# Kernel tuning notes

Measured on AMD Instinct MI355X. Metric: run time of the kernel, lower is better.

Reference implementation:

```python
import jax, jax.numpy as jnp
import numpy as np
import math

B, Q, H, KVH, D, KV, HID = 2, 1024, 32, 8, 128, 4096, 4096

def rotate_half(x):
    x1, x2 = jnp.split(x, 2, axis=-1)
    return jnp.concatenate([-x2, x1], axis=-1)

def setup_inputs() -> dict:
    key = jax.random.key(0)
    ks = jax.random.split(key, 10)
    inv = 1.0 / math.sqrt(HID)
    return {
        "hidden_states": jax.random.normal(ks[0], (B, Q, HID), dtype=jnp.float32),
        "cos": jax.random.uniform(ks[1], (B, 1, Q, D), dtype=jnp.float32),
        "sin": jax.random.uniform(ks[2], (B, 1, Q, D), dtype=jnp.float32),
        "attention_mask": jnp.zeros((B, 1, Q, KV), dtype=jnp.float32),
        "cache_k": jax.random.normal(ks[3], (B, KVH, KV, D), dtype=jnp.float32),
        "cache_v": jax.random.normal(ks[4], (B, KVH, KV, D), dtype=jnp.float32),
        "sink_ids": jnp.arange(Q, dtype=jnp.int32),
        "Wq": jax.random.normal(ks[5], (H * D, HID), dtype=jnp.float32) * inv,
        "Wk": jax.random.normal(ks[6], (KVH * D, HID), dtype=jnp.float32) * inv,
        "Wv": jax.random.normal(ks[7], (KVH * D, HID), dtype=jnp.float32) * inv,
        "Wo": jax.random.normal(ks[8], (HID, H * D), dtype=jnp.float32) * inv,
    }

def reference(hidden_states, cos, sin, attention_mask, cache_k, cache_v, sink_ids, Wq, Wk, Wv, Wo):
    b, q_len, hid = hidden_states.shape
    d = cos.shape[-1]
    h = Wq.shape[0] // d
    kvh = Wk.shape[0] // d
    n_rep = h // kvh

    # projections -> (b, heads, q, d)
    qs = (hidden_states @ Wq.T).reshape(b, q_len, h, d).transpose(0, 2, 1, 3)
    ks = (hidden_states @ Wk.T).reshape(b, q_len, kvh, d).transpose(0, 2, 1, 3)
    vs = (hidden_states @ Wv.T).reshape(b, q_len, kvh, d).transpose(0, 2, 1, 3)

    # RoPE
    qs = qs * cos + rotate_half(qs) * sin
    ks = ks * cos + rotate_half(ks) * sin

    # sink new K/V into the paged cache at sink_ids, then read back the full cache
    k_cache = cache_k.at[:, :, sink_ids, :].set(ks)
    v_cache = cache_v.at[:, :, sink_ids, :].set(vs)

    # repeat_kv: (b, kvh, kv, d) -> (b, h, kv, d)
    k_full = jnp.repeat(k_cache, n_rep, axis=1)
    v_full = jnp.repeat(v_cache, n_rep, axis=1)

    scores = jnp.einsum('bhqd,bhkd->bhqk', qs, k_full) / math.sqrt(d)
    scores = scores + attention_mask
    attn = jax.nn.softmax(scores.astype(jnp.float32), axis=-1).astype(qs.dtype)
    out = jnp.einsum('bhqk,bhkd->bhqd', attn, v_full)
    out = out.transpose(0, 2, 1, 3).reshape(b, q_len, h * d)
    return out @ Wo.T
```

## Files before the change

### kernel.cpp

```cpp
#include <hip/hip_runtime.h>

typedef __bf16 bf16;
typedef __attribute__((ext_vector_type(8))) __bf16 bf16x8;
typedef __attribute__((ext_vector_type(4))) __bf16 bf16x4;
typedef __attribute__((ext_vector_type(4))) float floatx4;

#define LOG2E 1.4426950408889634f
#define CEXP (0.08838834764831845f * 1.4426950408889634f)

__device__ __forceinline__ void lds16(const void* g, void* l) {
  __builtin_amdgcn_global_load_lds(
      (const __attribute__((address_space(1))) unsigned int*)(unsigned long long)g,
      (__attribute__((address_space(3))) unsigned int*)(unsigned int)(unsigned long long)l,
      16, 0, 0);
}

__device__ __forceinline__ void memfence() { asm volatile("" ::: "memory"); }

template <typename CT>
__global__ __launch_bounds__(256, 2) void gemm_bt(const bf16* __restrict__ A,
                                                  const bf16* __restrict__ W,
                                                  CT* __restrict__ C,
                                                  int M, int N, int K) {
  __shared__ bf16 sA[2][128 * 64];
  __shared__ bf16 sB[2][128 * 64];
  const int tid = threadIdx.x;
  const int lane = tid & 63;
  const int wave = tid >> 6;
  const int quad = lane >> 4;
  const int l16 = lane & 15;
  const int m0 = blockIdx.y * 128;
  const int n0 = blockIdx.x * 128;
  const int wm = (wave >> 1) * 64;
  const int wn = (wave & 1) * 64;

  floatx4 acc[4][4] = {};

  const int rsub = lane >> 3;
  const int csw = ((lane & 7) ^ rsub) * 8;
  const int NT = K >> 6;

  auto stage = [&](int buf, int t) {
    const int k0 = t << 6;
#pragma unroll
    for (int i = 0; i < 4; ++i) {
      const int row = i * 32 + wave * 8 + rsub;
      lds16(A + (long)(m0 + row) * K + k0 + csw, sA[buf] + (i * 32 + wave * 8) * 64);
      lds16(W + (long)(n0 + row) * K + k0 + csw, sB[buf] + (i * 32 + wave * 8) * 64);
    }
  };

  stage(0, 0);
  stage(1, 1);

  for (int t = 0; t < NT - 1; ++t) {
    const int buf = t & 1;
    asm volatile("s_waitcnt vmcnt(8)" ::: "memory");
    __builtin_amdgcn_s_barrier();
    memfence();
#pragma unroll
    for (int s = 0; s < 2; ++s) {
      bf16x8 af[4], bfr[4];
#pragma unroll
      for (int i = 0; i < 4; ++i)
        af[i] = *(const bf16x8*)(sA[buf] + (wm + i * 16 + l16) * 64 +
                                 (((s * 4 + quad) ^ (l16 & 7)) << 3));
#pragma unroll
      for (int j = 0; j < 4; ++j)
        bfr[j] = *(const bf16x8*)(sB[buf] + (wn + j * 16 + l16) * 64 +
                                  (((s * 4 + quad) ^ (l16 & 7)) << 3));
#pragma unroll
      for (int i = 0; i < 4; ++i)
#pragma unroll
        for (int j = 0; j < 4; ++j)
          acc[i][j] = __builtin_amdgcn_mfma_f32_16x16x32_bf16(af[i], bfr[j], acc[i][j], 0, 0, 0);
    }
    memfence();
    __builtin_amdgcn_s_barrier();
    memfence();
    if (t + 2 < NT) stage(buf, t + 2);
  }

  asm volatile("s_waitcnt vmcnt(0)" ::: "memory");
  __builtin_amdgcn_s_barrier();
  memfence();
  {
    const int buf = (NT - 1) & 1;
#pragma unroll
    for (int s = 0; s < 2; ++s) {
      bf16x8 af[4], bfr[4];
#pragma unroll
      for (int i = 0; i < 4; ++i)
        af[i] = *(const bf16x8*)(sA[buf] + (wm + i * 16 + l16) * 64 +
                                 (((s * 4 + quad) ^ (l16 & 7)) << 3));
#pragma unroll
      for (int j = 0; j < 4; ++j)
        bfr[j] = *(const bf16x8*)(sB[buf] + (wn + j * 16 + l16) * 64 +
                                  (((s * 4 + quad) ^ (l16 & 7)) << 3));
#pragma unroll
      for (int i = 0; i < 4; ++i)
#pragma unroll
        for (int j = 0; j < 4; ++j)
          acc[i][j] = __builtin_amdgcn_mfma_f32_16x16x32_bf16(af[i], bfr[j], acc[i][j], 0, 0, 0);
    }
  }

#pragma unroll
  for (int i = 0; i < 4; ++i) {
    const int row = m0 + wm + i * 16 + quad * 4;
#pragma unroll
    for (int j = 0; j < 4; ++j) {
      const int col = n0 + wn + j * 16 + l16;
#pragma unroll
      for (int r = 0; r < 4; ++r)
        C[(long)(row + r) * N + col] = (CT)acc[i][j][r];
    }
  }
}

__global__ __launch_bounds__(256, 2) void attn(const bf16* __restrict__ qr,
                                               const bf16* __restrict__ kc,
                                               const bf16* __restrict__ vt,
                                               const float* __restrict__ mask,
                                               const int* __restrict__ flag,
                                               bf16* __restrict__ o) {
  __shared__ bf16 sK[2][64 * 128];
  __shared__ bf16 sV[2][128 * 64];
  __shared__ bf16 sP[4 * 32 * 64];
  const int tid = threadIdx.x, lane = tid & 63, wave = tid >> 6;
  const int quad = lane >> 4, l16 = lane & 15;

  int id = blockIdx.x;
  const int kvh = id & 7;
  id >>= 3;
  const int b = id & 1;
  id >>= 1;
  const int h = kvh * 4 + (id & 3);
  const int q0 = (id >> 2) * 128;
  const int qw = q0 + wave * 32;

  const bf16* qbase = qr + ((long)(b * 32 + h) * 1024 + qw) * 128;
  bf16x8 qf[2][4];
#pragma unroll
  for (int qt = 0; qt < 2; ++qt)
#pragma unroll
    for (int ks = 0; ks < 4; ++ks)
      qf[qt][ks] = *(const bf16x8*)(qbase + (long)(qt * 16 + l16) * 128 +
                                    ks * 32 + quad * 8);

  floatx4 oacc[8][2] = {};
  floatx4 lrun4[2] = {};

  const bool use_mask = (*flag != 0);
  const bf16* kbase = kc + (long)(b * 8 + kvh) * 4096 * 128;
  const bf16* vbase = vt + (long)(b * 8 + kvh) * 128 * 4096;
  bf16* sPw = sP + wave * 2048;

  auto stage = [&](int buf, int kt) {
    const int kv0 = kt * 64;
#pragma unroll
    for (int it = 0; it < 4; ++it) {
      const int r0 = wave * 16 + it * 4;
      const int row = r0 + (lane >> 4);
      lds16(kbase + (long)(kv0 + row) * 128 + (((lane & 15) ^ (row & 15)) << 3),
            sK[buf] + r0 * 128);
    }
#pragma unroll
    for (int it = 0; it < 4; ++it) {
      const int r0 = wave * 32 + it * 8;
      const int row = r0 + (lane >> 3);
      lds16(vbase + (long)row * 4096 + kv0 + (((lane & 7) ^ (row & 7)) << 3),
            sV[buf] + r0 * 64);
    }
  };

  stage(0, 0);
  __syncthreads();

  for (int kt = 0; kt < 64; ++kt) {
    const int cur = kt & 1;
    const int kv0 = kt * 64;
    if (kt < 63) stage(cur ^ 1, kt + 1);

    floatx4 s[4][2] = {};
    __builtin_amdgcn_s_setprio(1);
#pragma unroll
    for (int ks = 0; ks < 4; ++ks)
#pragma unroll
      for (int j = 0; j < 4; ++j) {
        const bf16x8 kf = *(const bf16x8*)(sK[cur] + (j * 16 + l16) * 128 +
                                           (((ks * 4 + quad) ^ l16) << 3));
        s[j][0] = __builtin_amdgcn_mfma_f32_16x16x32_bf16(kf, qf[0][ks], s[j][0], 0, 0, 0);
        s[j][1] = __builtin_amdgcn_mfma_f32_16x16x32_bf16(kf, qf[1][ks], s[j][1], 0, 0, 0);
      }
    __builtin_amdgcn_s_setprio(0);

    if (use_mask) {
#pragma unroll
      for (int qt = 0; qt < 2; ++qt)
#pragma unroll
        for (int j = 0; j < 4; ++j)
#pragma unroll
          for (int r = 0; r < 4; ++r) {
            const int q = qw + qt * 16 + l16;
            const int kv = kv0 + j * 16 + quad * 4 + r;
            s[j][qt][r] += mask[((long)b * 1024 + q) * 4096 + kv] * LOG2E;
          }
    }

#pragma unroll
    for (int qt = 0; qt < 2; ++qt)
#pragma unroll
      for (int j = 0; j < 4; ++j) {
        bf16x4 pk;
        floatx4 pv;
#pragma unroll
        for (int r = 0; r < 4; ++r) {
          pv[r] = exp2f(s[j][qt][r]);
          pk[r] = (bf16)pv[r];
        }
        lrun4[qt] += pv;
        *(bf16x4*)(sPw + (qt * 16 + l16) * 64 +
                   (((j * 2 + (quad >> 1)) ^ (l16 & 7)) << 3) + ((quad & 1) << 2)) = pk;
      }

    __builtin_amdgcn_s_setprio(1);
#pragma unroll
    for (int kc2 = 0; kc2 < 2; ++kc2) {
      const int ph = ((kc2 * 4 + quad) ^ (l16 & 7)) << 3;
      const bf16x8 pf0 = *(const bf16x8*)(sPw + l16 * 64 + ph);
      const bf16x8 pf1 = *(const bf16x8*)(sPw + (16 + l16) * 64 + ph);
#pragma unroll
      for (int mt = 0; mt < 8; ++mt) {
        const bf16x8 vf = *(const bf16x8*)(sV[cur] + (mt * 16 + l16) * 64 + ph);
        oacc[mt][0] = __builtin_amdgcn_mfma_f32_16x16x32_bf16(vf, pf0, oacc[mt][0], 0, 0, 0);
        oacc[mt][1] = __builtin_amdgcn_mfma_f32_16x16x32_bf16(vf, pf1, oacc[mt][1], 0, 0, 0);
      }
    }
    __builtin_amdgcn_s_setprio(0);

    __syncthreads();
  }

#pragma unroll
  for (int qt = 0; qt < 2; ++qt) {
    float ls = (lrun4[qt][0] + lrun4[qt][1]) + (lrun4[qt][2] + lrun4[qt][3]);
    ls += __shfl_xor(ls, 16, 64);
    ls += __shfl_xor(ls, 32, 64);
    const float inv = 1.f / ls;
    const int q = qw + qt * 16 + l16;
    bf16* op = o + ((long)(b * 1024 + q) * 32 + h) * 128 + quad * 4;
#pragma unroll
    for (int mt = 0; mt < 8; ++mt) {
      bf16x4 ov;
#pragma unroll
      for (int r = 0; r < 4; ++r) ov[r] = (bf16)(oacc[mt][qt][r] * inv);
      *(bf16x4*)(op + mt * 16) = ov;
    }
  }
}

__global__ void zeroflag(int* f) { *f = 0; }

__global__ void prep(const floatx4* __restrict__ hid, const floatx4* __restrict__ wq,
                     const floatx4* __restrict__ wk, const floatx4* __restrict__ wv,
                     const floatx4* __restrict__ ck, const floatx4* __restrict__ mask,
                     bf16x4* __restrict__ hidb, bf16x4* __restrict__ wqkvb,
                     bf16x4* __restrict__ kcb, int* __restrict__ flag) {
  const int bid = blockIdx.x;
  const int tid = threadIdx.x;
  if (bid >= 40960) {
    const long i = (long)(bid - 40960) * 256 + tid;
    const floatx4 v = mask[i];
    if (v[0] != 0.f || v[1] != 0.f || v[2] != 0.f || v[3] != 0.f) atomicOr(flag, 1);
    return;
  }
  const floatx4* in;
  bf16x4* out;
  long i;
  if (bid < 8192)       { i = (long)bid * 256 + tid;           in = hid; out = hidb; }
  else if (bid < 24576) { i = (long)(bid - 8192) * 256 + tid;  in = wq;  out = wqkvb; }
  else if (bid < 28672) { i = (long)(bid - 24576) * 256 + tid; in = wk;  out = wqkvb + 4194304; }
  else if (bid < 32768) { i = (long)(bid - 28672) * 256 + tid; in = wv;  out = wqkvb + 5242880; }
  else                  { i = (long)(bid - 32768) * 256 + tid; in = ck;  out = kcb; }
  const floatx4 v = in[i];
  bf16x4 o;
  o[0] = (bf16)v[0]; o[1] = (bf16)v[1]; o[2] = (bf16)v[2]; o[3] = (bf16)v[3];
  out[i] = o;
}

__global__ void f2b4(const floatx4* __restrict__ in, bf16x4* __restrict__ out) {
  const long i = (long)blockIdx.x * 256 + threadIdx.x;
  const floatx4 v = in[i];
  bf16x4 o;
  o[0] = (bf16)v[0]; o[1] = (bf16)v[1]; o[2] = (bf16)v[2]; o[3] = (bf16)v[3];
  out[i] = o;
}

__global__ void vtrans(const float* __restrict__ v, bf16* __restrict__ vt) {
  __shared__ float t[64][33];
  const int bk = blockIdx.z;
  const int kv0 = blockIdx.x * 64, d0 = blockIdx.y * 32;
  const int tid = threadIdx.x;
  const float* src = v + ((long)bk * 4096 + kv0) * 128 + d0;
  const int rr = tid >> 5, cc = tid & 31;
#pragma unroll
  for (int p = 0; p < 8; ++p)
    t[p * 8 + rr][cc] = src[(long)(p * 8 + rr) * 128 + cc];
  __syncthreads();
  const int rowD = tid >> 3, oct = tid & 7;
  bf16x8 o;
#pragma unroll
  for (int i = 0; i < 8; ++i) o[i] = (bf16)t[oct * 8 + i][rowD];
  *(bf16x8*)(vt + ((long)bk * 128 + d0 + rowD) * 4096 + kv0 + oct * 8) = o;
}

__global__ void ropes(const bf16* __restrict__ qkv, const float* __restrict__ cosp,
                      const float* __restrict__ sinp, const int* __restrict__ sink,
                      bf16* __restrict__ qrope, bf16* __restrict__ kcb,
                      bf16* __restrict__ vtb) {
  const int bid = blockIdx.x;
  const int tid = threadIdx.x;
  if (bid < 4096) {
    const int t = bid * 256 + tid;
    const int j = t & 15;
    const int q = (t >> 4) & 1023;
    const int h = (t >> 14) & 31;
    const int b = t >> 19;
    const long qrow = ((long)b * 1024 + q) * 6144 + h * 128;
    const bf16x4 x = *(const bf16x4*)(qkv + qrow + j * 4);
    const bf16x4 y = *(const bf16x4*)(qkv + qrow + 64 + j * 4);
    const long ci = ((long)b * 1024 + q) * 128 + j * 4;
    const floatx4 cl = *(const floatx4*)(cosp + ci);
    const floatx4 sl = *(const floatx4*)(sinp + ci);
    const floatx4 ch = *(const floatx4*)(cosp + ci + 64);
    const floatx4 sh = *(const floatx4*)(sinp + ci + 64);
    bf16x4 xo, yo;
#pragma unroll
    for (int i = 0; i < 4; ++i) {
      const float xf = (float)x[i], yf = (float)y[i];
      xo[i] = (bf16)((xf * cl[i] - yf * sl[i]) * CEXP);
      yo[i] = (bf16)((yf * ch[i] + xf * sh[i]) * CEXP);
    }
    bf16* ob = qrope + ((long)(b * 32 + h) * 1024 + q) * 128 + j * 4;
    *(bf16x4*)ob = xo;
    *(bf16x4*)(ob + 64) = yo;
  } else if (bid < 5120) {
    const int t = (bid - 4096) * 256 + tid;
    const int j = t & 15;
    const int q = (t >> 4) & 1023;
    const int kvh = (t >> 14) & 7;
    const int b = t >> 17;
    const long krow = ((long)b * 1024 + q) * 6144 + 4096 + kvh * 128;
    const bf16x4 x = *(const bf16x4*)(qkv + krow + j * 4);
    const bf16x4 y = *(const bf16x4*)(qkv + krow + 64 + j * 4);
    const long ci = ((long)b * 1024 + q) * 128 + j * 4;
    const floatx4 cl = *(const floatx4*)(cosp + ci);
    const floatx4 sl = *(const floatx4*)(sinp + ci);
    const floatx4 ch = *(const floatx4*)(cosp + ci + 64);
    const floatx4 sh = *(const floatx4*)(sinp + ci + 64);
    bf16x4 xo, yo;
#pragma unroll
    for (int i = 0; i < 4; ++i) {
      const float xf = (float)x[i], yf = (float)y[i];
      xo[i] = (bf16)(xf * cl[i] - yf * sl[i]);
      yo[i] = (bf16)(yf * ch[i] + xf * sh[i]);
    }
    const int sk = sink[q];
    bf16* ob = kcb + (((long)b * 8 + kvh) * 4096 + sk) * 128 + j * 4;
    *(bf16x4*)ob = xo;
    *(bf16x4*)(ob + 64) = yo;
  } else {
    const int t = (bid - 5120) * 256 + tid;
    const int j = t & 15;
    const int q = (t >> 4) & 1023;
    const int kvh = (t >> 14) & 7;
    const int b = t >> 17;
    const bf16x8 v = *(const bf16x8*)(qkv + ((long)b * 1024 + q) * 6144 + 5120 +
                                      kvh * 128 + j * 8);
    const int sk = sink[q];
    bf16* dst = vtb + (((long)b * 8 + kvh) * 128 + j * 8) * 4096 + sk;
#pragma unroll
    for (int i = 0; i < 8; ++i) dst[(long)i * 4096] = v[i];
  }
}

extern "C" void kernel_launch(void* const* d_in, const int* in_sizes, int n_in,
                              void* d_out, int out_size, void* d_ws, size_t ws_size,
                              hipStream_t stream) {
  const float* hid  = (const float*)d_in[0];
  const float* cosp = (const float*)d_in[1];
  const float* sinp = (const float*)d_in[2];
  const float* mask = (const float*)d_in[3];
  const float* ck   = (const float*)d_in[4];
  const float* cv   = (const float*)d_in[5];
  const int*   sink = (const int*)d_in[6];
  const float* Wq   = (const float*)d_in[7];
  const float* Wk   = (const float*)d_in[8];
  const float* Wv   = (const float*)d_in[9];
  const float* Wo   = (const float*)d_in[10];
  float* out = (float*)d_out;

  char* ws = (char*)d_ws;
  bf16* wqkv  = (bf16*)(ws);
  bf16* hidb  = (bf16*)(ws + 50331648);
  bf16* qkvb  = (bf16*)(ws + 67108864);
  bf16* qrope = (bf16*)(ws + 92274688);
  bf16* kcb   = (bf16*)(ws + 109051904);
  bf16* vtb   = (bf16*)(ws + 125829120);
  bf16* ob    = (bf16*)(ws + 142606336);
  int*  flag  = (int*)(ws + 159383552);
  bf16* wob   = (bf16*)(ws + 50331648);

  zeroflag<<<1, 1, 0, stream>>>(flag);

  prep<<<49152, 256, 0, stream>>>((const floatx4*)hid, (const floatx4*)Wq,
                                  (const floatx4*)Wk, (const floatx4*)Wv,
                                  (const floatx4*)ck, (const floatx4*)mask,
                                  (bf16x4*)hidb, (bf16x4*)wqkv, (bf16x4*)kcb, flag);

  vtrans<<<dim3(64, 4, 16), 256, 0, stream>>>(cv, vtb);

  gemm_bt<bf16><<<dim3(48, 16), 256, 0, stream>>>(hidb, wqkv, qkvb, 2048, 6144, 4096);

  ropes<<<6144, 256, 0, stream>>>(qkvb, cosp, sinp, sink, qrope, kcb, vtb);

  f2b4<<<16384, 256, 0, stream>>>((const floatx4*)Wo, (bf16x4*)wob);

  attn<<<512, 256, 0, stream>>>(qrope, kcb, vtb, mask, flag, ob);

  gemm_bt<float><<<dim3(32, 16), 256, 0, stream>>>(ob, wob, out, 2048, 4096, 4096);

  (void)in_sizes; (void)n_in; (void)out_size; (void)ws_size;
}
```

Before: 629.2 us.

## Enlarge GEMM tiles to 256x256 with 8 waves and phased MFMA barriers

The bf16 GEMM moves from 128x128 tiles with 4 waves to 256x256 tiles with 8 waves, each wave computing 128x64. This raises reuse of each staged tile and cuts global loads per FLOP. The inner loop is split into four phases with barriers and s_setprio around the MFMA bursts so waves interleave LDS reads and matrix ops. The cost is far fewer blocks (192 and 128), which can underfill 256 CUs, plus 128KB of LDS per block and higher register pressure.

Result: slower. 702.2 us (+11.6%).

```diff
diff --git a/kernel.cpp b/kernel.cpp
--- a/kernel.cpp
+++ b/kernel.cpp
@@ -18,23 +18,23 @@
 __device__ __forceinline__ void memfence() { asm volatile("" ::: "memory"); }
 
 template <typename CT>
-__global__ __launch_bounds__(256, 2) void gemm_bt(const bf16* __restrict__ A,
+__global__ __launch_bounds__(512, 2) void gemm_bt(const bf16* __restrict__ A,
                                                   const bf16* __restrict__ W,
                                                   CT* __restrict__ C,
                                                   int M, int N, int K) {
-  __shared__ bf16 sA[2][128 * 64];
-  __shared__ bf16 sB[2][128 * 64];
+  __shared__ alignas(16) bf16 sA[2][256 * 64];
+  __shared__ alignas(16) bf16 sB[2][256 * 64];
   const int tid = threadIdx.x;
   const int lane = tid & 63;
   const int wave = tid >> 6;
   const int quad = lane >> 4;
   const int l16 = lane & 15;
-  const int m0 = blockIdx.y * 128;
-  const int n0 = blockIdx.x * 128;
-  const int wm = (wave >> 1) * 64;
-  const int wn = (wave & 1) * 64;
-
-  floatx4 acc[4][4] = {};
+  const int m0 = blockIdx.y * 256;
+  const int n0 = blockIdx.x * 256;
+  const int wm = (wave >> 2) * 128;
+  const int wn = (wave & 3) * 64;
+
+  floatx4 acc[8][4] = {};
 
   const int rsub = lane >> 3;
   const int csw = ((lane & 7) ^ rsub) * 8;
@@ -44,9 +44,40 @@
     const int k0 = t << 6;
 #pragma unroll
     for (int i = 0; i < 4; ++i) {
-      const int row = i * 32 + wave * 8 + rsub;
-      lds16(A + (long)(m0 + row) * K + k0 + csw, sA[buf] + (i * 32 + wave * 8) * 64);
-      lds16(W + (long)(n0 + row) * K + k0 + csw, sB[buf] + (i * 32 + wave * 8) * 64);
+      const int r0 = wave * 32 + i * 8;
+      const int row = r0 + rsub;
+      lds16(A + (long)(m0 + row) * K + k0 + csw, sA[buf] + r0 * 64);
+      lds16(W + (long)(n0 + row) * K + k0 + csw, sB[buf] + r0 * 64);
+    }
+  };
+
+  auto phases = [&](int buf) {
+    bf16x8 bfr[4];
+#pragma unroll
+    for (int p = 0; p < 4; ++p) {
+      const int ks = p >> 1, mg = p & 1;
+      if (mg == 0) {
+#pragma unroll
+        for (int j = 0; j < 4; ++j)
+          bfr[j] = *(const bf16x8*)(sB[buf] + (wn + j * 16 + l16) * 64 +
+                                    (((ks * 4 + quad) ^ (l16 & 7)) << 3));
+      }
+      bf16x8 af[4];
+#pragma unroll
+      for (int a = 0; a < 4; ++a)
+        af[a] = *(const bf16x8*)(sA[buf] + (wm + (mg * 4 + a) * 16 + l16) * 64 +
+                                 (((ks * 4 + quad) ^ (l16 & 7)) << 3));
+      __builtin_amdgcn_s_setprio(1);
+#pragma unroll
+      for (int a = 0; a < 4; ++a)
+#pragma unroll
+        for (int j = 0; j < 4; ++j)
+          acc[mg * 4 + a][j] =
+              __builtin_amdgcn_mfma_f32_16x16x32_bf16(af[a], bfr[j], acc[mg * 4 + a][j], 0, 0, 0);
+      __builtin_amdgcn_s_setprio(0);
+      memfence();
+      __builtin_amdgcn_s_barrier();
+      memfence();
     }
   };
 
@@ -58,55 +89,17 @@
     asm volatile("s_waitcnt vmcnt(8)" ::: "memory");
     __builtin_amdgcn_s_barrier();
     memfence();
-#pragma unroll
-    for (int s = 0; s < 2; ++s) {
-      bf16x8 af[4], bfr[4];
-#pragma unroll
-      for (int i = 0; i < 4; ++i)
-        af[i] = *(const bf16x8*)(sA[buf] + (wm + i * 16 + l16) * 64 +
-                                 (((s * 4 + quad) ^ (l16 & 7)) << 3));
-#pragma unroll
-      for (int j = 0; j < 4; ++j)
-        bfr[j] = *(const bf16x8*)(sB[buf] + (wn + j * 16 + l16) * 64 +
-                                  (((s * 4 + quad) ^ (l16 & 7)) << 3));
-#pragma unroll
-      for (int i = 0; i < 4; ++i)
-#pragma unroll
-        for (int j = 0; j < 4; ++j)
-          acc[i][j] = __builtin_amdgcn_mfma_f32_16x16x32_bf16(af[i], bfr[j], acc[i][j], 0, 0, 0);
-    }
-    memfence();
-    __builtin_amdgcn_s_barrier();
-    memfence();
+    phases(buf);
     if (t + 2 < NT) stage(buf, t + 2);
   }
 
   asm volatile("s_waitcnt vmcnt(0)" ::: "memory");
   __builtin_amdgcn_s_barrier();
   memfence();
-  {
-    const int buf = (NT - 1) & 1;
-#pragma unroll
-    for (int s = 0; s < 2; ++s) {
-      bf16x8 af[4], bfr[4];
-#pragma unroll
-      for (int i = 0; i < 4; ++i)
-        af[i] = *(const bf16x8*)(sA[buf] + (wm + i * 16 + l16) * 64 +
-                                 (((s * 4 + quad) ^ (l16 & 7)) << 3));
-#pragma unroll
-      for (int j = 0; j < 4; ++j)
-        bfr[j] = *(const bf16x8*)(sB[buf] + (wn + j * 16 + l16) * 64 +
-                                  (((s * 4 + quad) ^ (l16 & 7)) << 3));
-#pragma unroll
-      for (int i = 0; i < 4; ++i)
-#pragma unroll
-        for (int j = 0; j < 4; ++j)
-          acc[i][j] = __builtin_amdgcn_mfma_f32_16x16x32_bf16(af[i], bfr[j], acc[i][j], 0, 0, 0);
-    }
-  }
-
-#pragma unroll
-  for (int i = 0; i < 4; ++i) {
+  phases((NT - 1) & 1);
+
+#pragma unroll
+  for (int i = 0; i < 8; ++i) {
     const int row = m0 + wm + i * 16 + quad * 4;
 #pragma unroll
     for (int j = 0; j < 4; ++j) {
@@ -421,7 +414,7 @@
 
   vtrans<<<dim3(64, 4, 16), 256, 0, stream>>>(cv, vtb);
 
-  gemm_bt<bf16><<<dim3(48, 16), 256, 0, stream>>>(hidb, wqkv, qkvb, 2048, 6144, 4096);
+  gemm_bt<bf16><<<dim3(24, 8), 512, 0, stream>>>(hidb, wqkv, qkvb, 2048, 6144, 4096);
 
   ropes<<<6144, 256, 0, stream>>>(qkvb, cosp, sinp, sink, qrope, kcb, vtb);
 
@@ -429,7 +422,7 @@
 
   attn<<<512, 256, 0, stream>>>(qrope, kcb, vtb, mask, flag, ob);
 
-  gemm_bt<float><<<dim3(32, 16), 256, 0, stream>>>(ob, wob, out, 2048, 4096, 4096);
+  gemm_bt<float><<<dim3(16, 8), 512, 0, stream>>>(ob, wob, out, 2048, 4096, 4096);
 
   (void)in_sizes; (void)n_in; (void)out_size; (void)ws_size;
 }
```
